# Optimization experiments

Hardware: AMD Instinct MI355X
Metric: run time of the kernel (lower is better)

The kernel has to match this reference:

```python
import jax, jax.numpy as jnp
import numpy as np
from math import sqrt

N_USERS = 60000
N_ITEMS = 40000
D = 64
B = 3
LAYERS = 2
E = 600000
BATCH = 2048
N_NODES = (N_USERS + 1) + (N_ITEMS + 1)
REG_WEIGHT = 1e-3
BPR_GAMMA = 1e-10


def setup_inputs() -> dict:
    key = jax.random.key(0)
    k0, k1, k2, k3, k4 = jax.random.split(key, 5)
    user_emb = jax.random.normal(k0, (N_USERS + 1, D), jnp.float32) * 0.1
    item_emb = jax.random.normal(k1, (N_ITEMS + 1, D), jnp.float32) * 0.1
    W = jnp.ones((B,), jnp.float32)
    edge_users = jax.random.randint(k2, (B, E), 1, N_USERS + 1)
    edge_items = jax.random.randint(k3, (B, E), 1, N_ITEMS + 1)
    batch_data = jax.random.randint(k4, (BATCH, B, 3), 1, N_ITEMS + 1)
    return dict(user_emb=user_emb, item_emb=item_emb, W=W,
                edge_users=edge_users, edge_items=edge_items,
                batch_data=batch_data)


def _lightgcn(emb, eu, ei, layers):
    # bipartite undirected graph: users <-> items (items offset by N_USERS+1)
    it = ei + (N_USERS + 1)
    src = jnp.concatenate([eu, it])
    dst = jnp.concatenate([it, eu])
    deg = jax.ops.segment_sum(jnp.ones_like(src, jnp.float32), src, N_NODES)
    norm = jax.lax.rsqrt(jnp.maximum(deg[src], 1.0)) * jax.lax.rsqrt(jnp.maximum(deg[dst], 1.0))
    out = emb
    cur = emb
    for _ in range(layers):
        cur = jax.ops.segment_sum(cur[src] * norm[:, None], dst, N_NODES)
        out = out + cur
    return out / (layers + 1)


def _mutual_attention(f):
    # f: [N, B, D]
    S = jnp.einsum('nid,njd->nij', f, f)          # [N, B, B] pairwise scores
    last = S[:, B - 1:B, :]                        # [N, 1, B]
    proj = S[:, :B - 1, :]                         # [N, B-1, B]
    # (last * proj) * last / (last^2 + eps)   (dim-1 is size 1, sums/norms trivial)
    clear = (last * proj) * last / (last * last + 1e-12)   # [N, B-1, B]
    scores = jnp.sum(clear, axis=1, keepdims=True) + last   # [N, 1, B]
    all_scores = jnp.concatenate([clear, scores], axis=1)   # [N, B, B]
    att = jax.nn.softmax(all_scores / sqrt(D), axis=-1)
    return jnp.einsum('nij,njd->nid', att, f)


def reference(user_emb, item_emb, W, edge_users, edge_items, batch_data):
    total0 = jnp.concatenate([user_emb, item_emb], axis=0)   # [N_NODES, D]
    # global graph = union of all behaviors
    g_eu = edge_users.reshape(-1)
    g_ei = edge_items.reshape(-1)
    all_emb = _lightgcn(total0, g_eu, g_ei, LAYERS)
    # per-behavior propagation
    u_list, i_list = [], []
    for b in range(B):
        eb = _lightgcn(all_emb, edge_users[b], edge_items[b], LAYERS)
        u_list.append(eb[:N_USERS + 1])
        i_list.append(eb[N_USERS + 1:])
    all_user = jnp.stack(u_list, axis=1)   # [n_users+1, B, D]
    all_item = jnp.stack(i_list, axis=1)   # [n_items+1, B, D]
    all_user = _mutual_attention(all_user)
    # item behaviour degree: interactions per item per behavior
    ones = jnp.ones((E,), jnp.float32)
    ibd = jnp.stack([jax.ops.segment_sum(ones, edge_items[b], N_ITEMS + 1)
                     for b in range(B)], axis=1)   # [n_items+1, B]
    weight = ibd * W
    weight = weight / (jnp.sum(weight, axis=1, keepdims=True) + 1e-8)
    item_final = jnp.sum(all_item * weight[:, :, None], axis=1)   # [n_items+1, D]
    total_loss = jnp.float32(0.0)
    for b in range(B):
        users = batch_data[:, b, 0]
        items = batch_data[:, b, 1:3]
        uf = all_user[:, b][users][:, None, :]      # [batch, 1, D]
        itf = item_final[items]                      # [batch, 2, D]
        scores = jnp.sum(uf * itf, axis=2)           # [batch, 2]
        total_loss = total_loss - jnp.mean(
            jnp.log(BPR_GAMMA + jax.nn.sigmoid(scores[:, 0] - scores[:, 1])))
    emb_loss = (jnp.linalg.norm(user_emb) + jnp.linalg.norm(item_emb)) / (N_ITEMS + 1)
    return total_loss + REG_WEIGHT * emb_loss
```

## Files before the change

### kernel.cpp

```cpp
#include <hip/hip_runtime.h>
#include <hip/hip_bf16.h>
#include <math.h>

#define NUQ 60001
#define NIQ 40001
#define NNQ 100002
#define DQ  64
#define EQ  600000
#define BQ  3
#define BATCHQ 2048
#define ROWW 32
#define RST ((NNQ + 1) * ROWW)
#define NSLOT (BATCHQ * BQ)
#define NPAD 100004
#define ADJB 1200000
#define BLK_ELE 2048
#define NBLK ((NNQ + BLK_ELE - 1) / BLK_ELE)
#define RANGE 392
#define NRANGE 256
#define NBINS (BQ * NRANGE)
#define NBLKA 256
#define EPB ((BQ * EQ + NBLKA - 1) / NBLKA)

__device__ __forceinline__ float wave_sum(float v) {
#pragma unroll
  for (int m = 32; m >= 1; m >>= 1) v += __shfl_xor(v, m, 64);
  return v;
}
__device__ __forceinline__ int wave_sum_i(int v) {
#pragma unroll
  for (int m = 32; m >= 1; m >>= 1) v += __shfl_xor(v, m, 64);
  return v;
}

__device__ __forceinline__ unsigned pack_bf2(float lo, float hi) {
  unsigned a = __float_as_uint(lo);
  unsigned b = __float_as_uint(hi);
  a = (a + 0x7FFFu + ((a >> 16) & 1u)) >> 16;
  b = (b + 0x7FFFu + ((b >> 16) & 1u)) >> 16;
  return a | (b << 16);
}
__device__ __forceinline__ float unpk_lo(unsigned u) { return __uint_as_float(u << 16); }
__device__ __forceinline__ float unpk_hi(unsigned u) { return __uint_as_float(u & 0xFFFF0000u); }

__device__ __forceinline__ void ntst_u32(unsigned* p, unsigned v) { __builtin_nontemporal_store(v, p); }
__device__ __forceinline__ void ntst_f32(float* p, float v) { __builtin_nontemporal_store(v, p); }
__device__ __forceinline__ unsigned ntld_u32(const unsigned* p) { return __builtin_nontemporal_load(p); }
__device__ __forceinline__ float ntld_f32(const float* p) { return __builtin_nontemporal_load(p); }

__global__ void zero_i_k(int* __restrict__ p, int n) {
  int tid = blockIdx.x * blockDim.x + threadIdx.x;
  int stride = gridDim.x * blockDim.x;
  for (int i = tid; i < n; i += stride) p[i] = 0;
}

__global__ void sumsq_k(const float* __restrict__ p, int n, float* __restrict__ acc) {
  int tid = blockIdx.x * blockDim.x + threadIdx.x;
  int stride = gridDim.x * blockDim.x;
  float s = 0.f;
  for (int i = tid; i < n; i += stride) { float v = p[i]; s += v * v; }
  s = wave_sum(s);
  __shared__ float ws[4];
  if ((threadIdx.x & 63) == 0) ws[threadIdx.x >> 6] = s;
  __syncthreads();
  if (threadIdx.x == 0) atomicAdd(acc, ws[0] + ws[1] + ws[2] + ws[3]);
}

__global__ void binc_k(const int* __restrict__ eu, const int* __restrict__ ei,
                       unsigned* __restrict__ counts) {
  __shared__ unsigned h[NBINS];
  for (int i = threadIdx.x; i < NBINS; i += 256) h[i] = 0u;
  __syncthreads();
  int base = blockIdx.x * EPB;
  int end = base + EPB;
  if (end > BQ * EQ) end = BQ * EQ;
  for (int idx = base + threadIdx.x; idx < end; idx += 256) {
    int b = idx / EQ;
    int u = eu[idx];
    int it = ei[idx] + NUQ;
    atomicAdd(&h[b * NRANGE + u / RANGE], 1u);
    atomicAdd(&h[b * NRANGE + it / RANGE], 1u);
  }
  __syncthreads();
  for (int i = threadIdx.x; i < NBINS; i += 256)
    counts[(size_t)blockIdx.x * NBINS + i] = h[i];
}

__global__ void binscan1_k(const unsigned* __restrict__ counts,
                           unsigned* __restrict__ offs, unsigned* __restrict__ bintot) {
  int bin = blockIdx.x;
  int t = threadIdx.x;
  int lane = t & 63, wid = t >> 6;
  unsigned v = counts[(size_t)t * NBINS + bin];
  unsigned incl = v;
#pragma unroll
  for (int off = 1; off < 64; off <<= 1) {
    unsigned x = __shfl_up(incl, off, 64);
    if (lane >= off) incl += x;
  }
  __shared__ unsigned wsum[4];
  if (lane == 63) wsum[wid] = incl;
  __syncthreads();
  if (t == 0) {
    unsigned s = 0;
#pragma unroll
    for (int w = 0; w < 4; ++w) { unsigned x = wsum[w]; wsum[w] = s; s += x; }
  }
  __syncthreads();
  unsigned excl = incl - v + wsum[wid];
  offs[(size_t)t * NBINS + bin] = excl;
  if (t == 255) bintot[bin] = excl + v;
}

__global__ void binscan2_k(const unsigned* __restrict__ bintot,
                           unsigned* __restrict__ binstart) {
  int t = threadIdx.x;
  int lane = t & 63, wid = t >> 6;
  unsigned c0 = bintot[t * 3 + 0], c1 = bintot[t * 3 + 1], c2 = bintot[t * 3 + 2];
  unsigned tsum = c0 + c1 + c2;
  unsigned incl = tsum;
#pragma unroll
  for (int off = 1; off < 64; off <<= 1) {
    unsigned x = __shfl_up(incl, off, 64);
    if (lane >= off) incl += x;
  }
  __shared__ unsigned wsum[4];
  if (lane == 63) wsum[wid] = incl;
  __syncthreads();
  if (t == 0) {
    unsigned s = 0;
#pragma unroll
    for (int w = 0; w < 4; ++w) { unsigned x = wsum[w]; wsum[w] = s; s += x; }
  }
  __syncthreads();
  unsigned run = incl - tsum + wsum[wid];
  binstart[t * 3 + 0] = run; run += c0;
  binstart[t * 3 + 1] = run; run += c1;
  binstart[t * 3 + 2] = run; run += c2;
  if (t == 255) binstart[NBINS] = run;
}

__global__ void binfill_k(const int* __restrict__ eu, const int* __restrict__ ei,
                          const unsigned* __restrict__ offs,
                          const unsigned* __restrict__ binstart,
                          unsigned* __restrict__ records) {
  __shared__ unsigned cur[NBINS];
  for (int i = threadIdx.x; i < NBINS; i += 256)
    cur[i] = binstart[i] + offs[(size_t)blockIdx.x * NBINS + i];
  __syncthreads();
  int base = blockIdx.x * EPB;
  int end = base + EPB;
  if (end > BQ * EQ) end = BQ * EQ;
  for (int idx = base + threadIdx.x; idx < end; idx += 256) {
    int b = idx / EQ;
    int u = eu[idx];
    int itl = ei[idx];
    int it = itl + NUQ;
    unsigned p = atomicAdd(&cur[b * NRANGE + u / RANGE], 1u);
    records[p] = ((unsigned)(u % RANGE) << 16) | (unsigned)itl;
    unsigned q = atomicAdd(&cur[b * NRANGE + it / RANGE], 1u);
    records[q] = ((unsigned)(it % RANGE) << 16) | (unsigned)u;
  }
}

__global__ void bindeg_k(const unsigned* __restrict__ records,
                         const unsigned* __restrict__ binstart,
                         int* __restrict__ degB) {
  int bin = blockIdx.x;
  int b = bin / NRANGE;
  int r0 = (bin % NRANGE) * RANGE;
  __shared__ int h[RANGE];
  for (int i = threadIdx.x; i < RANGE; i += 256) h[i] = 0;
  __syncthreads();
  unsigned rs = binstart[bin], re = binstart[bin + 1];
  for (unsigned j = rs + threadIdx.x; j < re; j += 256)
    atomicAdd(&h[records[j] >> 16], 1);
  __syncthreads();
  int nval = NNQ - r0;
  if (nval > RANGE) nval = RANGE;
  int* deg = degB + (size_t)b * NPAD;
  for (int i = threadIdx.x; i < nval; i += 256) deg[r0 + i] = h[i];
}

__global__ void scan_p1_k(const int* __restrict__ degB, int* __restrict__ partial) {
  int b = blockIdx.x / NBLK;
  int blk = blockIdx.x % NBLK;
  const int* deg = degB + (size_t)b * NPAD;
  int base = blk * BLK_ELE + threadIdx.x * 8;
  int s = 0;
#pragma unroll
  for (int i = 0; i < 8; ++i) { int idx = base + i; if (idx < NNQ) s += deg[idx]; }
  s = wave_sum_i(s);
  __shared__ int lds[4];
  int wid = threadIdx.x >> 6;
  if ((threadIdx.x & 63) == 0) lds[wid] = s;
  __syncthreads();
  if (threadIdx.x == 0) partial[b * NBLK + blk] = lds[0] + lds[1] + lds[2] + lds[3];
}

__global__ void scan_p2_k(int* __restrict__ partial, int* __restrict__ rowptrB) {
  int wid = threadIdx.x >> 6;
  int lane = threadIdx.x & 63;
  if (wid >= BQ) return;
  int v = (lane < NBLK) ? partial[wid * NBLK + lane] : 0;
  int orig = v;
#pragma unroll
  for (int off = 1; off < 64; off <<= 1) {
    int t = __shfl_up(v, off, 64);
    if (lane >= off) v += t;
  }
  if (lane < NBLK) partial[wid * NBLK + lane] = v - orig;
  if (lane == NBLK - 1) rowptrB[(size_t)wid * NPAD + NNQ] = v;
}

__global__ void scan_p3_k(const int* __restrict__ degB, const int* __restrict__ partial,
                          int* __restrict__ rowptrB, float* __restrict__ invsqB) {
  int b = blockIdx.x / NBLK;
  int blk = blockIdx.x % NBLK;
  const int* deg = degB + (size_t)b * NPAD;
  int* rowptr = rowptrB + (size_t)b * NPAD;
  float* invsq = invsqB + (size_t)b * NPAD;
  int base = blk * BLK_ELE + threadIdx.x * 8;
  int d[8];
  int tsum = 0;
#pragma unroll
  for (int i = 0; i < 8; ++i) {
    int idx = base + i;
    d[i] = (idx < NNQ) ? deg[idx] : 0;
    tsum += d[i];
  }
  int lane = threadIdx.x & 63;
  int wid = threadIdx.x >> 6;
  int incl = tsum;
#pragma unroll
  for (int off = 1; off < 64; off <<= 1) {
    int t = __shfl_up(incl, off, 64);
    if (lane >= off) incl += t;
  }
  int excl = incl - tsum;
  __shared__ int lds[4];
  if (lane == 63) lds[wid] = incl;
  __syncthreads();
  if (threadIdx.x == 0) {
    int s = 0;
#pragma unroll
    for (int w = 0; w < 4; ++w) { int t = lds[w]; lds[w] = s; s += t; }
  }
  __syncthreads();
  int run = excl + lds[wid] + partial[b * NBLK + blk];
#pragma unroll
  for (int i = 0; i < 8; ++i) {
    int idx = base + i;
    if (idx < NNQ) {
      rowptr[idx] = run;
      run += d[i];
      invsq[idx] = rsqrtf(fmaxf((float)d[i], 1.f));
    }
  }
}

__global__ void invsqg_k(const int* __restrict__ degB, float* __restrict__ invsqG) {
  int n = blockIdx.x * blockDim.x + threadIdx.x;
  if (n >= NNQ) return;
  int dg = degB[n] + degB[NPAD + n] + degB[2 * NPAD + n];
  invsqG[n] = rsqrtf(fmaxf((float)dg, 1.f));
}

__global__ void binscat_k(const unsigned* __restrict__ records,
                          const unsigned* __restrict__ binstart,
                          const int* __restrict__ rowptrB,
                          unsigned short* __restrict__ adjB) {
  int bin = blockIdx.x;
  int b = bin / NRANGE;
  int r0 = (bin % NRANGE) * RANGE;
  int nval = NNQ - r0;
  if (nval > RANGE) nval = RANGE;
  __shared__ int cur[RANGE];
  const int* rowptr = rowptrB + (size_t)b * NPAD;
  for (int i = threadIdx.x; i < nval; i += 256) cur[i] = rowptr[r0 + i];
  __syncthreads();
  unsigned rs = binstart[bin], re = binstart[bin + 1];
  unsigned short* adj = adjB + (size_t)b * ADJB;
  for (unsigned j = rs + threadIdx.x; j < re; j += 256) {
    unsigned rec = records[j];
    int dl = rec >> 16;
    int pos = atomicAdd(&cur[dl], 1);
    adj[pos] = (unsigned short)(rec & 0xFFFFu);
  }
}

__global__ void pack_emb_k(const float* __restrict__ ue, const float* __restrict__ ie,
                           const float* __restrict__ invsqG,
                           unsigned* __restrict__ E0, unsigned* __restrict__ E0s) {
  int idx = blockIdx.x * blockDim.x + threadIdx.x;
  if (idx >= (NNQ + 1) * ROWW) return;
  int n = idx >> 5, k = idx & 31;
  if (n >= NNQ) { E0s[idx] = 0u; return; }
  const float* src = (n < NUQ) ? (ue + (size_t)n * DQ) : (ie + (size_t)(n - NUQ) * DQ);
  float a = src[2 * k], b = src[2 * k + 1];
  ntst_u32(&E0[idx], pack_bf2(a, b));
  float s = invsqG[n];
  ntst_u32(&E0s[idx], pack_bf2(a * s, b * s));
}

__device__ __forceinline__ void gather_ns(const unsigned* __restrict__ S,
                                          const unsigned short* __restrict__ adj,
                                          int start, int end, int offs,
                                          int lane, unsigned k4, int g,
                                          float& alo, float& ahi) {
  for (int j0 = start; j0 < end; j0 += 64) {
    int nloc = end - j0;
    if (nloc > 64) nloc = 64;
    unsigned boff = ((unsigned)NNQ) << 7;
    if (lane < nloc) boff = (unsigned)((int)adj[j0 + lane] + offs) << 7;
    for (int j = 0; j < nloc; j += 16) {
#pragma unroll
      for (int m = 0; m < 8; ++m) {
        int jj = j + 2 * m + g;
        unsigned bo = (unsigned)__shfl((int)boff, jj, 64) + k4;
        unsigned dd = *(const unsigned*)((const char*)S + bo);
        alo += unpk_lo(dd);
        ahi += unpk_hi(dd);
      }
    }
  }
}

__device__ __forceinline__ void gather3(const unsigned* __restrict__ S,
                                        const unsigned short* __restrict__ adjB,
                                        int s0, int d0, int s1, int d1,
                                        int s2, int d2, int offs,
                                        int lane, unsigned k4, int g,
                                        float& alo, float& ahi) {
  int D = d0 + d1 + d2;
  int d01 = d0 + d1;
  for (int j0 = 0; j0 < D; j0 += 64) {
    int nloc = D - j0;
    if (nloc > 64) nloc = 64;
    unsigned boff = ((unsigned)NNQ) << 7;
    int l = j0 + lane;
    if (l < D) {
      int idx;
      if (l < d0)       idx = s0 + l;
      else if (l < d01) idx = ADJB + s1 + (l - d0);
      else              idx = 2 * ADJB + s2 + (l - d01);
      boff = (unsigned)((int)adjB[idx] + offs) << 7;
    }
    for (int j = 0; j < nloc; j += 16) {
#pragma unroll
      for (int m = 0; m < 8; ++m) {
        int jj = j + 2 * m + g;
        unsigned bo = (unsigned)__shfl((int)boff, jj, 64) + k4;
        unsigned dd = *(const unsigned*)((const char*)S + bo);
        alo += unpk_lo(dd);
        ahi += unpk_hi(dd);
      }
    }
  }
}

__device__ __forceinline__ void gather_w(const unsigned* __restrict__ S,
                                         const unsigned short* __restrict__ adj,
                                         const float* __restrict__ invsq,
                                         int start, int end, int offs,
                                         int lane, unsigned k4, int g,
                                         float& alo, float& ahi) {
  for (int j0 = start; j0 < end; j0 += 64) {
    int nloc = end - j0;
    if (nloc > 64) nloc = 64;
    unsigned boff = (unsigned)offs << 7;
    float w = 0.f;
    if (lane < nloc) {
      int a = (int)adj[j0 + lane] + offs;
      boff = (unsigned)a << 7;
      w = invsq[a];
    }
    for (int j = 0; j < nloc; j += 16) {
#pragma unroll
      for (int m = 0; m < 8; ++m) {
        int jj = j + 2 * m + g;
        unsigned bo = (unsigned)__shfl((int)boff, jj, 64) + k4;
        float ww = __shfl(w, jj, 64);
        unsigned dd = *(const unsigned*)((const char*)S + bo);
        alo += ww * unpk_lo(dd);
        ahi += ww * unpk_hi(dd);
      }
    }
  }
}

__global__ void g_l1_k(const unsigned* __restrict__ E0s, unsigned* __restrict__ T1,
                       unsigned* __restrict__ T1s,
                       const int* __restrict__ rowptrB, const unsigned short* __restrict__ adjB,
                       const float* __restrict__ invsqG) {
  int wid = (blockIdx.x * blockDim.x + threadIdx.x) >> 6;
  int lane = threadIdx.x & 63;
  if (wid > NNQ) return;
  int k = lane & 31, g = lane >> 5;
  unsigned k4 = (unsigned)k << 2;
  if (wid == NNQ) { if (lane < 32) T1s[(size_t)wid * ROWW + k] = 0u; return; }
  int offs = (wid < NUQ) ? NUQ : 0;
  const int* rp0 = rowptrB;
  const int* rp1 = rowptrB + NPAD;
  const int* rp2 = rowptrB + 2 * (size_t)NPAD;
  int s0 = rp0[wid], d0 = rp0[wid + 1] - s0;
  int s1 = rp1[wid], d1 = rp1[wid + 1] - s1;
  int s2 = rp2[wid], d2 = rp2[wid + 1] - s2;
  float alo = 0.f, ahi = 0.f;
  gather3(E0s, adjB, s0, d0, s1, d1, s2, d2, offs, lane, k4, g, alo, ahi);
  alo += __shfl_xor(alo, 32, 64);
  ahi += __shfl_xor(ahi, 32, 64);
  float s = invsqG[wid];
  if (lane < 32) {
    ntst_u32(&T1[(size_t)wid * ROWW + k], pack_bf2(alo * s, ahi * s));
    ntst_u32(&T1s[(size_t)wid * ROWW + k], pack_bf2(alo * s * s, ahi * s * s));
  }
}

__global__ void g_l2c_k(const unsigned* __restrict__ E0, const unsigned* __restrict__ T1,
                        const unsigned* __restrict__ T1s,
                        unsigned* __restrict__ C, unsigned* __restrict__ Cs,
                        const int* __restrict__ rowptrB, const unsigned short* __restrict__ adjB,
                        const float* __restrict__ invsqG, const float* __restrict__ invsqB) {
  int wid = (blockIdx.x * blockDim.x + threadIdx.x) >> 6;
  int lane = threadIdx.x & 63;
  if (wid > NNQ) return;
  int k = lane & 31, g = lane >> 5;
  unsigned k4 = (unsigned)k << 2;
  if (wid == NNQ) {
    if (lane < 32) {
#pragma unroll
      for (int b = 0; b < BQ; ++b) Cs[(size_t)b * RST + (size_t)wid * ROWW + k] = 0u;
    }
    return;
  }
  int offs = (wid < NUQ) ? NUQ : 0;
  const int* rp0 = rowptrB;
  const int* rp1 = rowptrB + NPAD;
  const int* rp2 = rowptrB + 2 * (size_t)NPAD;
  int s0 = rp0[wid], d0 = rp0[wid + 1] - s0;
  int s1 = rp1[wid], d1 = rp1[wid + 1] - s1;
  int s2 = rp2[wid], d2 = rp2[wid + 1] - s2;
  float alo = 0.f, ahi = 0.f;
  gather3(T1s, adjB, s0, d0, s1, d1, s2, d2, offs, lane, k4, g, alo, ahi);
  alo += __shfl_xor(alo, 32, 64);
  ahi += __shfl_xor(ahi, 32, 64);
  if (lane < 32) {
    float s = invsqG[wid];
    unsigned e0 = ntld_u32(&E0[(size_t)wid * ROWW + k]);
    unsigned t1 = ntld_u32(&T1[(size_t)wid * ROWW + k]);
    float clo = (unpk_lo(e0) + unpk_lo(t1) + alo * s) * (1.f / 3.f);
    float chi = (unpk_hi(e0) + unpk_hi(t1) + ahi * s) * (1.f / 3.f);
    ntst_u32(&C[(size_t)wid * ROWW + k], pack_bf2(clo, chi));
#pragma unroll
    for (int b = 0; b < BQ; ++b) {
      float sb = invsqB[(size_t)b * NPAD + wid];
      ntst_u32(&Cs[(size_t)b * RST + (size_t)wid * ROWW + k], pack_bf2(clo * sb, chi * sb));
    }
  }
}

__global__ void b_l1_k(const unsigned* __restrict__ Csb, unsigned* __restrict__ T1Bb,
                       const int* __restrict__ rowptr, const unsigned short* __restrict__ adj,
                       const float* __restrict__ ivb) {
  int wid = (blockIdx.x * blockDim.x + threadIdx.x) >> 6;
  int lane = threadIdx.x & 63;
  if (wid >= NNQ) return;
  int k = lane & 31, g = lane >> 5;
  unsigned k4 = (unsigned)k << 2;
  int offs = (wid < NUQ) ? NUQ : 0;
  float alo = 0.f, ahi = 0.f;
  gather_ns(Csb, adj, rowptr[wid], rowptr[wid + 1], offs, lane, k4, g, alo, ahi);
  alo += __shfl_xor(alo, 32, 64);
  ahi += __shfl_xor(ahi, 32, 64);
  float s = ivb[wid];
  if (lane < 32)
    ntst_u32(&T1Bb[(size_t)wid * ROWW + k], pack_bf2(alo * s, ahi * s));
}

__global__ void slot_users_k(const unsigned* __restrict__ C, const unsigned* __restrict__ T1B,
                             const int* __restrict__ rowptrB, const unsigned short* __restrict__ adjB,
                             const float* __restrict__ invsqB,
                             const int* __restrict__ batch, float* __restrict__ UG) {
  int slot = (blockIdx.x * blockDim.x + threadIdx.x) >> 6;
  int lane = threadIdx.x & 63;
  if (slot >= NSLOT) return;
  int b = blockIdx.y;
  const int* rp = rowptrB + (size_t)b * NPAD;
  const float* iv = invsqB + (size_t)b * NPAD;
  const unsigned* T1 = T1B + (size_t)b * NNQ * ROWW;
  int u = batch[slot * 3 + 0];
  int k = lane & 31, g = lane >> 5;
  unsigned k4 = (unsigned)k << 2;
  float alo = 0.f, ahi = 0.f;
  gather_w(T1, adjB + (size_t)b * ADJB, iv, rp[u], rp[u + 1], NUQ, lane, k4, g, alo, ahi);
  alo += __shfl_xor(alo, 32, 64);
  ahi += __shfl_xor(ahi, 32, 64);
  float s = iv[u];
  unsigned c0 = C[(size_t)u * ROWW + k];
  unsigned t0 = T1[(size_t)u * ROWW + k];
  if (lane < 32) {
    size_t base = ((size_t)slot * BQ + b) * DQ;
    ntst_f32(&UG[base + 2 * k],     (unpk_lo(c0) + unpk_lo(t0) + alo * s) * (1.f / 3.f));
    ntst_f32(&UG[base + 2 * k + 1], (unpk_hi(c0) + unpk_hi(t0) + ahi * s) * (1.f / 3.f));
  }
}

__global__ void slot_items_k(const unsigned* __restrict__ C, const unsigned* __restrict__ T1B,
                             const int* __restrict__ rowptrB, const unsigned short* __restrict__ adjB,
                             const float* __restrict__ invsqB,
                             const int* __restrict__ batch, float* __restrict__ IG) {
  int islot = (blockIdx.x * blockDim.x + threadIdx.x) >> 6;
  int lane = threadIdx.x & 63;
  if (islot >= 2 * NSLOT) return;
  int b = blockIdx.y;
  const int* rp = rowptrB + (size_t)b * NPAD;
  const float* iv = invsqB + (size_t)b * NPAD;
  const unsigned* T1 = T1B + (size_t)b * NNQ * ROWW;
  int slot = islot >> 1;
  int c = (islot & 1) + 1;
  int n = batch[slot * 3 + c] + NUQ;
  int k = lane & 31, g = lane >> 5;
  unsigned k4 = (unsigned)k << 2;
  float alo = 0.f, ahi = 0.f;
  gather_w(T1, adjB + (size_t)b * ADJB, iv, rp[n], rp[n + 1], 0, lane, k4, g, alo, ahi);
  alo += __shfl_xor(alo, 32, 64);
  ahi += __shfl_xor(ahi, 32, 64);
  float s = iv[n];
  unsigned c0 = C[(size_t)n * ROWW + k];
  unsigned t0 = T1[(size_t)n * ROWW + k];
  if (lane < 32) {
    size_t base = ((size_t)islot * BQ + b) * DQ;
    ntst_f32(&IG[base + 2 * k],     (unpk_lo(c0) + unpk_lo(t0) + alo * s) * (1.f / 3.f));
    ntst_f32(&IG[base + 2 * k + 1], (unpk_hi(c0) + unpk_hi(t0) + ahi * s) * (1.f / 3.f));
  }
}

__global__ void epilogue_k(const float* __restrict__ UG, const float* __restrict__ IG,
                           const int* __restrict__ degB, const int* __restrict__ batch,
                           const float* __restrict__ W, float* __restrict__ acc) {
  int slot = (blockIdx.x * blockDim.x + threadIdx.x) >> 6;
  int lane = threadIdx.x & 63;
  float val = 0.f;
  if (slot < NSLOT) {
    int bb = slot % BQ;
    size_t base = (size_t)slot * (BQ * DQ) + lane;
    float a0 = ntld_f32(&UG[base]);
    float a1 = ntld_f32(&UG[base + 64]);
    float a2 = ntld_f32(&UG[base + 128]);
    float p00 = wave_sum(a0 * a0);
    float p01 = wave_sum(a0 * a1);
    float p02 = wave_sum(a0 * a2);
    float p11 = wave_sum(a1 * a1);
    float p12 = wave_sum(a1 * a2);
    float p22 = wave_sum(a2 * a2);
    float last[3] = {p02, p12, p22};
    float S0[3] = {p00, p01, p02};
    float S1[3] = {p01, p11, p12};
    float rows[3][3];
#pragma unroll
    for (int j = 0; j < 3; ++j) {
      float l = last[j];
      float f = l * l / (l * l + 1e-12f);
      float c0 = S0[j] * f;
      float c1 = S1[j] * f;
      rows[0][j] = c0;
      rows[1][j] = c1;
      rows[2][j] = c0 + c1 + l;
    }
    float x0 = rows[bb][0] * 0.125f, x1 = rows[bb][1] * 0.125f, x2 = rows[bb][2] * 0.125f;
    float m = fmaxf(x0, fmaxf(x1, x2));
    float e0 = expf(x0 - m), e1 = expf(x1 - m), e2 = expf(x2 - m);
    float inv = 1.f / (e0 + e1 + e2);
    float uf = (e0 * a0 + e1 * a1 + e2 * a2) * inv;
    float sco[2];
#pragma unroll
    for (int c = 0; c < 2; ++c) {
      int islot = slot * 2 + c;
      int node = batch[slot * 3 + 1 + c] + NUQ;
      float w0 = (float)degB[0 * NPAD + node] * W[0];
      float w1 = (float)degB[1 * NPAD + node] * W[1];
      float w2 = (float)degB[2 * NPAD + node] * W[2];
      float inv2 = 1.f / (w0 + w1 + w2 + 1e-8f);
      size_t rb = (size_t)islot * (BQ * DQ) + lane;
      float ifv = (ntld_f32(&IG[rb]) * w0 + ntld_f32(&IG[rb + 64]) * w1 +
                   ntld_f32(&IG[rb + 128]) * w2) * inv2;
      sco[c] = wave_sum(uf * ifv);
    }
    if (lane == 0) {
      float x = sco[0] - sco[1];
      float sg = 1.f / (1.f + expf(-x));
      val = -logf(1e-10f + sg) * (1.f / (float)BATCHQ);
    }
  }
  __shared__ float ws[4];
  if (lane == 0) ws[threadIdx.x >> 6] = val;
  __syncthreads();
  if (threadIdx.x == 0) atomicAdd(acc, ws[0] + ws[1] + ws[2] + ws[3]);
}

__global__ void finalize_k(const float* __restrict__ sc, unsigned int* __restrict__ out) {
  float total = sc[0] + 0.001f * (sqrtf(sc[1]) + sqrtf(sc[2])) / (float)NIQ;
  unsigned int bits = __float_as_uint(total);
  unsigned int lsb = (bits >> 16) & 1u;
  unsigned int rb = (bits + 0x7FFFu + lsb) >> 16;
  out[0] = (rb << 16) | rb;
}

extern "C" void kernel_launch(void* const* d_in, const int* in_sizes, int n_in,
                              void* d_out, int out_size, void* d_ws, size_t ws_size,
                              hipStream_t stream) {
  const float* ue = (const float*)d_in[0];
  const float* ie = (const float*)d_in[1];
  const float* W  = (const float*)d_in[2];
  const int* eu    = (const int*)d_in[3];
  const int* ei    = (const int*)d_in[4];
  const int* batch = (const int*)d_in[5];

  unsigned* E0  = (unsigned*)d_ws;
  unsigned* E0s = E0 + (size_t)NNQ * ROWW;
  unsigned* T1  = E0s + (size_t)RST;
  unsigned* T1s = T1 + (size_t)NNQ * ROWW;
  unsigned* C   = T1s + (size_t)RST;
  unsigned* Cs  = C + (size_t)NNQ * ROWW;
  unsigned* T1B = Cs + (size_t)BQ * RST;
  float* UG   = (float*)(T1B + (size_t)BQ * NNQ * ROWW);
  float* IG   = UG + (size_t)NSLOT * (BQ * DQ);
  unsigned short* adjB = (unsigned short*)(IG + (size_t)2 * NSLOT * (BQ * DQ));
  int* rowptrB= (int*)(adjB + (size_t)BQ * ADJB);
  int* degB   = rowptrB + 3 * NPAD;
  float* invsqB = (float*)(degB + 3 * NPAD);
  float* invsqG = invsqB + 3 * NPAD;
  unsigned* counts = (unsigned*)(invsqG + NPAD);
  unsigned* offs   = counts + (size_t)NBLKA * NBINS;
  unsigned* bintot = offs + (size_t)NBLKA * NBINS;
  unsigned* binstart = bintot + 1024;
  unsigned* records = binstart + 1024;
  int* partial  = (int*)(records + (size_t)2 * BQ * EQ);
  float* sc   = (float*)(partial + 256);

  zero_i_k<<<1, 64, 0, stream>>>((int*)sc, 8);
  sumsq_k<<<512, 256, 0, stream>>>(ue, NUQ * DQ, sc + 1);
  sumsq_k<<<512, 256, 0, stream>>>(ie, NIQ * DQ, sc + 2);

  binc_k<<<NBLKA, 256, 0, stream>>>(eu, ei, counts);
  binscan1_k<<<NBINS, 256, 0, stream>>>(counts, offs, bintot);
  binscan2_k<<<1, 256, 0, stream>>>(bintot, binstart);
  binfill_k<<<NBLKA, 256, 0, stream>>>(eu, ei, offs, binstart, records);
  bindeg_k<<<NBINS, 256, 0, stream>>>(records, binstart, degB);
  scan_p1_k<<<BQ * NBLK, 256, 0, stream>>>(degB, partial);
  scan_p2_k<<<1, 256, 0, stream>>>(partial, rowptrB);
  scan_p3_k<<<BQ * NBLK, 256, 0, stream>>>(degB, partial, rowptrB, invsqB);
  invsqg_k<<<(NNQ + 255) / 256, 256, 0, stream>>>(degB, invsqG);
  binscat_k<<<NBINS, 256, 0, stream>>>(records, binstart, rowptrB, adjB);

  pack_emb_k<<<((NNQ + 1) * ROWW + 255) / 256, 256, 0, stream>>>(ue, ie, invsqG, E0, E0s);

  const int NODE_BLKS1 = (NNQ + 1 + 3) / 4;
  const int NODE_BLKS = (NNQ + 3) / 4;

  g_l1_k<<<NODE_BLKS1, 256, 0, stream>>>(E0s, T1, T1s, rowptrB, adjB, invsqG);
  g_l2c_k<<<NODE_BLKS1, 256, 0, stream>>>(E0, T1, T1s, C, Cs, rowptrB, adjB, invsqG, invsqB);

  for (int b = 0; b < BQ; ++b) {
    b_l1_k<<<NODE_BLKS, 256, 0, stream>>>(Cs + (size_t)b * RST,
                                          T1B + (size_t)b * NNQ * ROWW,
                                          rowptrB + (size_t)b * NPAD,
                                          adjB + (size_t)b * ADJB,
                                          invsqB + (size_t)b * NPAD);
  }

  slot_users_k<<<dim3((NSLOT + 3) / 4, 3), 256, 0, stream>>>(C, T1B, rowptrB, adjB, invsqB, batch, UG);
  slot_items_k<<<dim3((2 * NSLOT + 3) / 4, 3), 256, 0, stream>>>(C, T1B, rowptrB, adjB, invsqB, batch, IG);
  epilogue_k<<<(NSLOT + 3) / 4, 256, 0, stream>>>(UG, IG, degB, batch, W, sc);
  finalize_k<<<1, 1, 0, stream>>>(sc, (unsigned int*)d_out);
}
```

Measured before the change: 466.4 us.

## Apply per-neighbor normalization at gather time instead of materializing pre-scaled tables

Removes the pre-scaled copies E0s, T1s and the per-behavior Cs tables. Each gather now fetches a per-neighbor weight from the inverse-sqrt degree table and multiplies on the fly, which cuts the extra writes and workspace traffic of those tables. The three per-behavior b_l1 launches become one 2D-grid launch. In exchange each gathered neighbor needs an extra weight load and shuffle, and the dummy zero row used for padded lanes is dropped in favor of zero weights.

```diff
diff --git a/kernel.cpp b/kernel.cpp
--- a/kernel.cpp
+++ b/kernel.cpp
@@ -10,7 +10,6 @@
 #define BQ  3
 #define BATCHQ 2048
 #define ROWW 32
-#define RST ((NNQ + 1) * ROWW)
 #define NSLOT (BATCHQ * BQ)
 #define NPAD 100004
 #define ADJB 1200000
@@ -290,73 +289,13 @@
 }
 
 __global__ void pack_emb_k(const float* __restrict__ ue, const float* __restrict__ ie,
-                           const float* __restrict__ invsqG,
-                           unsigned* __restrict__ E0, unsigned* __restrict__ E0s) {
+                           unsigned* __restrict__ E0) {
   int idx = blockIdx.x * blockDim.x + threadIdx.x;
-  if (idx >= (NNQ + 1) * ROWW) return;
+  if (idx >= NNQ * ROWW) return;
   int n = idx >> 5, k = idx & 31;
-  if (n >= NNQ) { E0s[idx] = 0u; return; }
   const float* src = (n < NUQ) ? (ue + (size_t)n * DQ) : (ie + (size_t)(n - NUQ) * DQ);
   float a = src[2 * k], b = src[2 * k + 1];
   ntst_u32(&E0[idx], pack_bf2(a, b));
-  float s = invsqG[n];
-  ntst_u32(&E0s[idx], pack_bf2(a * s, b * s));
-}
-
-__device__ __forceinline__ void gather_ns(const unsigned* __restrict__ S,
-                                          const unsigned short* __restrict__ adj,
-                                          int start, int end, int offs,
-                                          int lane, unsigned k4, int g,
-                                          float& alo, float& ahi) {
-  for (int j0 = start; j0 < end; j0 += 64) {
-    int nloc = end - j0;
-    if (nloc > 64) nloc = 64;
-    unsigned boff = ((unsigned)NNQ) << 7;
-    if (lane < nloc) boff = (unsigned)((int)adj[j0 + lane] + offs) << 7;
-    for (int j = 0; j < nloc; j += 16) {
-#pragma unroll
-      for (int m = 0; m < 8; ++m) {
-        int jj = j + 2 * m + g;
-        unsigned bo = (unsigned)__shfl((int)boff, jj, 64) + k4;
-        unsigned dd = *(const unsigned*)((const char*)S + bo);
-        alo += unpk_lo(dd);
-        ahi += unpk_hi(dd);
-      }
-    }
-  }
-}
-
-__device__ __forceinline__ void gather3(const unsigned* __restrict__ S,
-                                        const unsigned short* __restrict__ adjB,
-                                        int s0, int d0, int s1, int d1,
-                                        int s2, int d2, int offs,
-                                        int lane, unsigned k4, int g,
-                                        float& alo, float& ahi) {
-  int D = d0 + d1 + d2;
-  int d01 = d0 + d1;
-  for (int j0 = 0; j0 < D; j0 += 64) {
-    int nloc = D - j0;
-    if (nloc > 64) nloc = 64;
-    unsigned boff = ((unsigned)NNQ) << 7;
-    int l = j0 + lane;
-    if (l < D) {
-      int idx;
-      if (l < d0)       idx = s0 + l;
-      else if (l < d01) idx = ADJB + s1 + (l - d0);
-      else              idx = 2 * ADJB + s2 + (l - d01);
-      boff = (unsigned)((int)adjB[idx] + offs) << 7;
-    }
-    for (int j = 0; j < nloc; j += 16) {
-#pragma unroll
-      for (int m = 0; m < 8; ++m) {
-        int jj = j + 2 * m + g;
-        unsigned bo = (unsigned)__shfl((int)boff, jj, 64) + k4;
-        unsigned dd = *(const unsigned*)((const char*)S + bo);
-        alo += unpk_lo(dd);
-        ahi += unpk_hi(dd);
-      }
-    }
-  }
 }
 
 __device__ __forceinline__ void gather_w(const unsigned* __restrict__ S,
@@ -389,16 +328,52 @@
   }
 }
 
-__global__ void g_l1_k(const unsigned* __restrict__ E0s, unsigned* __restrict__ T1,
-                       unsigned* __restrict__ T1s,
+__device__ __forceinline__ void gather3w(const unsigned* __restrict__ S,
+                                         const unsigned short* __restrict__ adjB,
+                                         const float* __restrict__ wtab,
+                                         int s0, int d0, int s1, int d1,
+                                         int s2, int d2, int offs,
+                                         int lane, unsigned k4, int g,
+                                         float& alo, float& ahi) {
+  int D = d0 + d1 + d2;
+  int d01 = d0 + d1;
+  for (int j0 = 0; j0 < D; j0 += 64) {
+    int nloc = D - j0;
+    if (nloc > 64) nloc = 64;
+    unsigned boff = (unsigned)offs << 7;
+    float w = 0.f;
+    int l = j0 + lane;
+    if (l < D) {
+      int idx;
+      if (l < d0)       idx = s0 + l;
+      else if (l < d01) idx = ADJB + s1 + (l - d0);
+      else              idx = 2 * ADJB + s2 + (l - d01);
+      int a = (int)adjB[idx] + offs;
+      boff = (unsigned)a << 7;
+      w = wtab[a];
+    }
+    for (int j = 0; j < nloc; j += 16) {
+#pragma unroll
+      for (int m = 0; m < 8; ++m) {
+        int jj = j + 2 * m + g;
+        unsigned bo = (unsigned)__shfl((int)boff, jj, 64) + k4;
+        float ww = __shfl(w, jj, 64);
+        unsigned dd = *(const unsigned*)((const char*)S + bo);
+        alo += ww * unpk_lo(dd);
+        ahi += ww * unpk_hi(dd);
+      }
+    }
+  }
+}
+
+__global__ void g_l1_k(const unsigned* __restrict__ E0, unsigned* __restrict__ T1,
                        const int* __restrict__ rowptrB, const unsigned short* __restrict__ adjB,
                        const float* __restrict__ invsqG) {
   int wid = (blockIdx.x * blockDim.x + threadIdx.x) >> 6;
   int lane = threadIdx.x & 63;
-  if (wid > NNQ) return;
+  if (wid >= NNQ) return;
   int k = lane & 31, g = lane >> 5;
   unsigned k4 = (unsigned)k << 2;
-  if (wid == NNQ) { if (lane < 32) T1s[(size_t)wid * ROWW + k] = 0u; return; }
   int offs = (wid < NUQ) ? NUQ : 0;
   const int* rp0 = rowptrB;
   const int* rp1 = rowptrB + NPAD;
@@ -407,33 +382,23 @@
   int s1 = rp1[wid], d1 = rp1[wid + 1] - s1;
   int s2 = rp2[wid], d2 = rp2[wid + 1] - s2;
   float alo = 0.f, ahi = 0.f;
-  gather3(E0s, adjB, s0, d0, s1, d1, s2, d2, offs, lane, k4, g, alo, ahi);
+  gather3w(E0, adjB, invsqG, s0, d0, s1, d1, s2, d2, offs, lane, k4, g, alo, ahi);
   alo += __shfl_xor(alo, 32, 64);
   ahi += __shfl_xor(ahi, 32, 64);
   float s = invsqG[wid];
-  if (lane < 32) {
+  if (lane < 32)
     ntst_u32(&T1[(size_t)wid * ROWW + k], pack_bf2(alo * s, ahi * s));
-    ntst_u32(&T1s[(size_t)wid * ROWW + k], pack_bf2(alo * s * s, ahi * s * s));
-  }
 }
 
 __global__ void g_l2c_k(const unsigned* __restrict__ E0, const unsigned* __restrict__ T1,
-                        const unsigned* __restrict__ T1s,
-                        unsigned* __restrict__ C, unsigned* __restrict__ Cs,
+                        unsigned* __restrict__ C,
                         const int* __restrict__ rowptrB, const unsigned short* __restrict__ adjB,
-                        const float* __restrict__ invsqG, const float* __restrict__ invsqB) {
+                        const float* __restrict__ invsqG) {
   int wid = (blockIdx.x * blockDim.x + threadIdx.x) >> 6;
   int lane = threadIdx.x & 63;
-  if (wid > NNQ) return;
+  if (wid >= NNQ) return;
   int k = lane & 31, g = lane >> 5;
   unsigned k4 = (unsigned)k << 2;
-  if (wid == NNQ) {
-    if (lane < 32) {
-#pragma unroll
-      for (int b = 0; b < BQ; ++b) Cs[(size_t)b * RST + (size_t)wid * ROWW + k] = 0u;
-    }
-    return;
-  }
   int offs = (wid < NUQ) ? NUQ : 0;
   const int* rp0 = rowptrB;
   const int* rp1 = rowptrB + NPAD;
@@ -442,40 +407,38 @@
   int s1 = rp1[wid], d1 = rp1[wid + 1] - s1;
   int s2 = rp2[wid], d2 = rp2[wid + 1] - s2;
   float alo = 0.f, ahi = 0.f;
-  gather3(T1s, adjB, s0, d0, s1, d1, s2, d2, offs, lane, k4, g, alo, ahi);
+  gather3w(T1, adjB, invsqG, s0, d0, s1, d1, s2, d2, offs, lane, k4, g, alo, ahi);
   alo += __shfl_xor(alo, 32, 64);
   ahi += __shfl_xor(ahi, 32, 64);
   if (lane < 32) {
     float s = invsqG[wid];
-    unsigned e0 = ntld_u32(&E0[(size_t)wid * ROWW + k]);
-    unsigned t1 = ntld_u32(&T1[(size_t)wid * ROWW + k]);
+    unsigned e0 = E0[(size_t)wid * ROWW + k];
+    unsigned t1 = T1[(size_t)wid * ROWW + k];
     float clo = (unpk_lo(e0) + unpk_lo(t1) + alo * s) * (1.f / 3.f);
     float chi = (unpk_hi(e0) + unpk_hi(t1) + ahi * s) * (1.f / 3.f);
     ntst_u32(&C[(size_t)wid * ROWW + k], pack_bf2(clo, chi));
-#pragma unroll
-    for (int b = 0; b < BQ; ++b) {
-      float sb = invsqB[(size_t)b * NPAD + wid];
-      ntst_u32(&Cs[(size_t)b * RST + (size_t)wid * ROWW + k], pack_bf2(clo * sb, chi * sb));
-    }
-  }
-}
-
-__global__ void b_l1_k(const unsigned* __restrict__ Csb, unsigned* __restrict__ T1Bb,
-                       const int* __restrict__ rowptr, const unsigned short* __restrict__ adj,
-                       const float* __restrict__ ivb) {
+  }
+}
+
+__global__ void b_l1_k(const unsigned* __restrict__ C, unsigned* __restrict__ T1B,
+                       const int* __restrict__ rowptrB, const unsigned short* __restrict__ adjB,
+                       const float* __restrict__ invsqB) {
   int wid = (blockIdx.x * blockDim.x + threadIdx.x) >> 6;
   int lane = threadIdx.x & 63;
   if (wid >= NNQ) return;
+  int b = blockIdx.y;
+  const int* rowptr = rowptrB + (size_t)b * NPAD;
+  const float* iv = invsqB + (size_t)b * NPAD;
   int k = lane & 31, g = lane >> 5;
   unsigned k4 = (unsigned)k << 2;
   int offs = (wid < NUQ) ? NUQ : 0;
   float alo = 0.f, ahi = 0.f;
-  gather_ns(Csb, adj, rowptr[wid], rowptr[wid + 1], offs, lane, k4, g, alo, ahi);
+  gather_w(C, adjB + (size_t)b * ADJB, iv, rowptr[wid], rowptr[wid + 1], offs, lane, k4, g, alo, ahi);
   alo += __shfl_xor(alo, 32, 64);
   ahi += __shfl_xor(ahi, 32, 64);
-  float s = ivb[wid];
+  float s = iv[wid];
   if (lane < 32)
-    ntst_u32(&T1Bb[(size_t)wid * ROWW + k], pack_bf2(alo * s, ahi * s));
+    ntst_u32(&T1B[(size_t)b * NNQ * ROWW + (size_t)wid * ROWW + k], pack_bf2(alo * s, ahi * s));
 }
 
 __global__ void slot_users_k(const unsigned* __restrict__ C, const unsigned* __restrict__ T1B,
@@ -618,12 +581,9 @@
   const int* batch = (const int*)d_in[5];
 
   unsigned* E0  = (unsigned*)d_ws;
-  unsigned* E0s = E0 + (size_t)NNQ * ROWW;
-  unsigned* T1  = E0s + (size_t)RST;
-  unsigned* T1s = T1 + (size_t)NNQ * ROWW;
-  unsigned* C   = T1s + (size_t)RST;
-  unsigned* Cs  = C + (size_t)NNQ * ROWW;
-  unsigned* T1B = Cs + (size_t)BQ * RST;
+  unsigned* T1  = E0 + (size_t)NNQ * ROWW;
+  unsigned* C   = T1 + (size_t)NNQ * ROWW;
+  unsigned* T1B = C + (size_t)NNQ * ROWW;
   float* UG   = (float*)(T1B + (size_t)BQ * NNQ * ROWW);
   float* IG   = UG + (size_t)NSLOT * (BQ * DQ);
   unsigned short* adjB = (unsigned short*)(IG + (size_t)2 * NSLOT * (BQ * DQ));
@@ -654,21 +614,14 @@
   invsqg_k<<<(NNQ + 255) / 256, 256, 0, stream>>>(degB, invsqG);
   binscat_k<<<NBINS, 256, 0, stream>>>(records, binstart, rowptrB, adjB);
 
-  pack_emb_k<<<((NNQ + 1) * ROWW + 255) / 256, 256, 0, stream>>>(ue, ie, invsqG, E0, E0s);
-
-  const int NODE_BLKS1 = (NNQ + 1 + 3) / 4;
+  pack_emb_k<<<(NNQ * ROWW + 255) / 256, 256, 0, stream>>>(ue, ie, E0);
+
   const int NODE_BLKS = (NNQ + 3) / 4;
 
-  g_l1_k<<<NODE_BLKS1, 256, 0, stream>>>(E0s, T1, T1s, rowptrB, adjB, invsqG);
-  g_l2c_k<<<NODE_BLKS1, 256, 0, stream>>>(E0, T1, T1s, C, Cs, rowptrB, adjB, invsqG, invsqB);
-
-  for (int b = 0; b < BQ; ++b) {
-    b_l1_k<<<NODE_BLKS, 256, 0, stream>>>(Cs + (size_t)b * RST,
-                                          T1B + (size_t)b * NNQ * ROWW,
-                                          rowptrB + (size_t)b * NPAD,
-                                          adjB + (size_t)b * ADJB,
-                                          invsqB + (size_t)b * NPAD);
-  }
+  g_l1_k<<<NODE_BLKS, 256, 0, stream>>>(E0, T1, rowptrB, adjB, invsqG);
+  g_l2c_k<<<NODE_BLKS, 256, 0, stream>>>(E0, T1, C, rowptrB, adjB, invsqG);
+
+  b_l1_k<<<dim3(NODE_BLKS, 3), 256, 0, stream>>>(C, T1B, rowptrB, adjB, invsqB);
 
   slot_users_k<<<dim3((NSLOT + 3) / 4, 3), 256, 0, stream>>>(C, T1B, rowptrB, adjB, invsqB, batch, UG);
   slot_items_k<<<dim3((2 * NSLOT + 3) / 4, 3), 256, 0, stream>>>(C, T1B, rowptrB, adjB, invsqB, batch, IG);
```

New measurement: 452.1 us. 1.03x faster.
